# Optimization experiments

Hardware: AMD Instinct MI355X
Metric: run time of the kernel (lower is better)

## Reference

```python
import jax, jax.numpy as jnp
import numpy as np

N_REACHES = 4096
N_STEPS = 96
DT = 3600.0  # routing timestep (s), default from MuskingumCungeRouter


def safe_pow(base, exp, eps=1e-6):
    # AD-safe power: exp(e * log(max(b, eps)))
    return jnp.exp(exp * jnp.log(jnp.maximum(base, eps)))


def setup_inputs() -> dict:
    key = jax.random.key(0)
    ks = jax.random.split(key, 10)
    n, T = N_REACHES, N_STEPS
    u = lambda k, lo, hi, shape: jax.random.uniform(k, shape, minval=lo, maxval=hi)
    lateral_inflows = u(ks[0], 0.0, 5.0, (T, n))          # m^3/s lateral inflow
    initial_Q = u(ks[1], 0.1, 10.0, (n,))
    lengths = u(ks[2], 500.0, 10000.0, (n,))              # reach length (m)
    slopes = u(ks[3], 1e-4, 0.05, (n,))                   # bed slope
    manning_n = u(ks[4], 0.02, 0.08, (n,))
    width_coef = u(ks[5], 2.0, 10.0, (n,))
    width_exp = u(ks[6], 0.4, 0.6, (n,))                  # ~0.5 typical
    depth_coef = u(ks[7], 0.2, 0.6, (n,))
    depth_exp = u(ks[8], 0.25, 0.35, (n,))                # ~0.3 typical
    # Strictly lower-triangular sparse adjacency: reach i receives from j < i
    # (valid topological order), ~4 upstream links per reach on average.
    upstream_mask = jnp.tril(jax.random.uniform(ks[9], (n, n)) < (4.0 / n), k=-1)
    is_outlet = jnp.arange(n) == n - 1
    return dict(lateral_inflows=lateral_inflows, initial_Q=initial_Q,
                lengths=lengths, slopes=slopes, manning_n=manning_n,
                width_coef=width_coef, width_exp=width_exp,
                depth_coef=depth_coef, depth_exp=depth_exp,
                upstream_mask=upstream_mask, is_outlet=is_outlet)


def _mc_coeffs(Q, L, S, mn, wc, we, dc, de, dt):
    """Vectorized Muskingum-Cunge coefficients for all reaches.

    Faithful fusion of compute_channel_geometry -> compute_velocity_manning ->
    compute_celerity -> compute_muskingum_params. Q here is Q_ref = max(state.Q, 0.1),
    which only depends on the previous state, so hoisting out of the per-reach
    scan is mathematically identical to the original.
    """
    Qs = jnp.maximum(Q, 0.01)
    W = wc * safe_pow(Qs, we)
    D = dc * safe_pow(Qs, de)
    A = W * D
    R = A / (W + 2.0 * D)                      # hydraulic radius
    safe_S = jnp.maximum(S, 1e-6)
    V = (1.0 / jnp.maximum(mn, 1e-3)) * safe_pow(R, 2.0 / 3.0) * jnp.sqrt(safe_S)
    c = jnp.maximum((5.0 / 3.0) * V, 0.01)     # kinematic wave celerity
    K = jnp.maximum(L / c, dt * 0.1)
    X = jnp.clip(0.5 * (1.0 - Q / (W * c * safe_S * L + 1e-6)), 0.0, 0.5)
    den = 2.0 * K * (1.0 - X) + dt
    C0 = jnp.maximum((dt - 2.0 * K * X) / den, 0.0)
    C1 = jnp.maximum((dt + 2.0 * K * X) / den, 0.0)
    C2 = jnp.maximum((2.0 * K * (1.0 - X) - dt) / den, 0.0)
    tot = C0 + C1 + C2
    return C0 / tot, C1 / tot, C2 / tot


def _route(lateral_inflows, initial_Q, lengths, slopes, manning_n,
           width_coef, width_exp, depth_coef, depth_exp,
           upstream_mask, is_outlet, dt=DT):
    n = lengths.shape[0]

    def step(state, lateral):
        Q, Q_prev, I_prev = state
        Q_ref = jnp.maximum(Q, 0.1)
        C0, C1, C2 = _mc_coeffs(Q_ref, lengths, slopes, manning_n,
                                width_coef, width_exp, depth_coef, depth_exp, dt)

        # Sequential topological sweep: masked reduction over already-routed reaches.
        def process(Q_acc, i):
            upstream_Q = jnp.sum(jnp.where(upstream_mask[i], Q_acc, 0.0))
            I_curr = upstream_Q + lateral[i]
            Q_out = jnp.maximum(C0[i] * I_curr + C1[i] * I_prev[i] + C2[i] * Q_prev[i], 0.0)
            return Q_acc.at[i].set(Q_out), I_curr

        Q_final, I_all = jax.lax.scan(process, jnp.zeros(n, lateral.dtype), jnp.arange(n))
        outlet_Q = jnp.sum(jnp.where(is_outlet, Q_final, 0.0))
        return (Q_final, Q, I_all), outlet_Q

    init = (initial_Q, initial_Q, jnp.zeros(n, initial_Q.dtype))
    _, outlet_series = jax.lax.scan(step, init, lateral_inflows)
    return outlet_series  # [n_timesteps]


def reference(lateral_inflows, initial_Q, lengths, slopes, manning_n,
              width_coef, width_exp, depth_coef, depth_exp,
              upstream_mask, is_outlet):
    return _route(lateral_inflows, initial_Q, lengths, slopes, manning_n,
                  width_coef, width_exp, depth_coef, depth_exp,
                  upstream_mask, is_outlet)
```

## Files before the change

### kernel.cpp

```cpp
#include <hip/hip_runtime.h>

#define NR 4096
#define NT 96
#define NNZ_CAP 10240
#define SREM_CAP 4096
#define LONG_CAP 4096
#define WLDS 8
#define SSTR 4112
#define DHIST 32
#define DTSTEP 3600.0f
#define LOG2_1E6 -19.931568f

__device__ __forceinline__ float RCP(float x) { return __builtin_amdgcn_rcpf(x); }
__device__ __forceinline__ float EXP2(float x) { return __builtin_amdgcn_exp2f(x); }
__device__ __forceinline__ float LOG2(float x) { return __builtin_amdgcn_logf(x); }

__device__ __forceinline__ void phase_barrier() {
  asm volatile("s_waitcnt lgkmcnt(0) vmcnt(6)" ::: "memory");
  __builtin_amdgcn_s_barrier();
  asm volatile("" ::: "memory");
}

__global__ void mc_build(const int* __restrict__ mask, int* __restrict__ rowBase,
                         int* __restrict__ rowCnt, int* __restrict__ gctr,
                         unsigned short* __restrict__ cols) {
  __shared__ unsigned short tmp[80];
  __shared__ int baseS;
  int row = blockIdx.x;
  int lane = threadIdx.x;
  const int* rs = mask + (size_t)row * NR;
  int total = 0;
  for (int j0 = 0; j0 < NR; j0 += 64) {
    int j = j0 + lane;
    int pred = (rs[j] != 0);
    unsigned long long m = __ballot(pred);
    if (pred) {
      int pos = total + __popcll(m & ((1ull << lane) - 1ull));
      if (pos < 80) tmp[pos] = (unsigned short)j;
    }
    total += __popcll(m);
  }
  if (total > 80) total = 80;
  if (lane == 0) {
    int b = atomicAdd(gctr, total);
    rowBase[row] = b;
    rowCnt[row] = total;
    baseS = b;
  }
  __syncthreads();
  int base = baseS;
  for (int e = lane; e < total; e += 64) {
    int p = base + e;
    if (p < NNZ_CAP) cols[p] = tmp[e];
  }
}

__global__ __launch_bounds__(1024) void mc_prep(
    const int* __restrict__ rowBase, const int* __restrict__ rowCnt,
    const int* __restrict__ gctr, const unsigned short* __restrict__ colsOld,
    unsigned short* __restrict__ orderG, unsigned short* __restrict__ levNG,
    unsigned short* __restrict__ scolG, unsigned int* __restrict__ sremMeta,
    unsigned int* __restrict__ longMeta, unsigned short* __restrict__ sremG,
    unsigned short* __restrict__ longG, unsigned char* __restrict__ lsG,
    int* __restrict__ meta) {
  __shared__ unsigned short cols_s[NNZ_CAP];
  __shared__ unsigned char lev_s[NR];
  __shared__ unsigned short newid_s[NR];
  __shared__ unsigned short order_s[NR];
  __shared__ unsigned char lsrc_s[NR];
  __shared__ int cnt[1024];
  __shared__ int sbuf[1024];
  __shared__ int maxLevS, flagS;
  const int tid = threadIdx.x;
  int nnz = gctr[0];
  if (nnz > NNZ_CAP) nnz = NNZ_CAP;
  for (int e = tid; e < nnz; e += 1024) cols_s[e] = colsOld[e];

  int b_r[4], e_r[4];
#pragma unroll
  for (int k = 0; k < 4; ++k) {
    int i = 4 * tid + k;
    int b = rowBase[i];
    if (b > NNZ_CAP) b = NNZ_CAP;
    int e = b + rowCnt[i];
    if (e > NNZ_CAP) e = NNZ_CAP;
    b_r[k] = b;
    e_r[k] = e;
    lev_s[i] = 0;
    lsrc_s[i] = 0;
  }
  if (tid == 0) maxLevS = 0;
  __syncthreads();

  for (int pass = 0; pass < 48; ++pass) {
    if (tid == 0) flagS = 0;
    __syncthreads();
    int ch = 0;
#pragma unroll
    for (int k = 0; k < 4; ++k) {
      int i = 4 * tid + k;
      int lv = 0;
      for (int e = b_r[k]; e < e_r[k]; ++e) {
        int l2 = (int)lev_s[cols_s[e]] + 1;
        lv = lv > l2 ? lv : l2;
      }
      if (lv > 127) lv = 127;
      if (lv > (int)lev_s[i]) {
        lev_s[i] = (unsigned char)lv;
        ch = 1;
      }
    }
    if (ch) flagS = 1;
    __syncthreads();
    int done = (flagS == 0);
    __syncthreads();
    if (done) break;
  }
  int lm = 0;
#pragma unroll
  for (int k = 0; k < 4; ++k) {
    int l = lev_s[4 * tid + k];
    lm = lm > l ? lm : l;
  }
  atomicMax(&maxLevS, lm);
  __syncthreads();
  const int maxLev = maxLevS;
  if (tid == 0) {
    meta[0] = maxLev + 1;
    meta[2] = (maxLev >= DHIST) ? 1 : 0;
  }
  if (maxLev >= DHIST) {
#pragma unroll
    for (int k = 0; k < 4; ++k) {
      int i = 4 * tid + k;
      orderG[i] = (unsigned short)i;
      levNG[i] = (unsigned short)lev_s[i];
    }
    return;
  }

  cnt[tid] = 0;
  __syncthreads();
  int bkt_r[4];
#pragma unroll
  for (int k = 0; k < 4; ++k) {
    int i = 4 * tid + k;
    int d = e_r[k] - b_r[k];
    if (d > 31) d = 31;
    int bkt = ((int)lev_s[i]) * 32 + d;
    bkt_r[k] = bkt;
    atomicAdd(&cnt[bkt], 1);
  }
  __syncthreads();
  int v = cnt[tid];
  sbuf[tid] = v;
  __syncthreads();
  for (int off = 1; off < 1024; off <<= 1) {
    int add = tid >= off ? sbuf[tid - off] : 0;
    __syncthreads();
    sbuf[tid] += add;
    __syncthreads();
  }
  cnt[tid] = sbuf[tid] - v;
  __syncthreads();
#pragma unroll
  for (int k = 0; k < 4; ++k) {
    int i = 4 * tid + k;
    int pos = atomicAdd(&cnt[bkt_r[k]], 1);
    order_s[pos] = (unsigned short)i;
    newid_s[i] = (unsigned short)pos;
  }
  __syncthreads();

#pragma unroll
  for (int k = 0; k < 4; ++k) {
    int p = 4 * tid + k;
    int oldi = order_s[p];
    orderG[p] = (unsigned short)oldi;
    int lp = (int)lev_s[oldi];
    levNG[p] = (unsigned short)lp;
    int b = rowBase[oldi];
    if (b > NNZ_CAP) b = NNZ_CAP;
    int e = b + rowCnt[oldi];
    if (e > NNZ_CAP) e = NNZ_CAP;
    int nS = 0, nR = 0, nL = 0;
    for (int ee = b; ee < e; ++ee) {
      int lag = lp - (int)lev_s[cols_s[ee]];
      if (lag < WLDS) {
        if (nS < 4) ++nS; else ++nR;
      } else ++nL;
    }
    if (nR > 63) nR = 63;
    if (nL > 63) nL = 63;
    int sB = nR ? atomicAdd(&meta[4], nR) : 0;
    int lB = nL ? atomicAdd(&meta[5], nL) : 0;
    if (sB > SREM_CAP) sB = SREM_CAP;
    if (sB + nR > SREM_CAP) nR = SREM_CAP - sB;
    if (lB > LONG_CAP) lB = LONG_CAP;
    if (lB + nL > LONG_CAP) nL = LONG_CAP - lB;
    unsigned short sc[4] = {4096, 4096, 4096, 4096};
    int iS = 0, cR = 0, cL = 0;
    for (int ee = b; ee < e; ++ee) {
      int cOld = cols_s[ee];
      int cN = newid_s[cOld];
      int lag = lp - (int)lev_s[cOld];
      if (lag < WLDS) {
        if (iS < 4) sc[iS++] = (unsigned short)cN;
        else if (cR < nR) { sremG[sB + cR] = (unsigned short)cN; ++cR; }
      } else {
        if (cL < nL) { longG[lB + cL] = (unsigned short)cN; ++cL; }
        lsrc_s[cN] = 1;
      }
    }
    scolG[4 * p + 0] = sc[0];
    scolG[4 * p + 1] = sc[1];
    scolG[4 * p + 2] = sc[2];
    scolG[4 * p + 3] = sc[3];
    sremMeta[p] = (unsigned)sB | ((unsigned)nR << 20) | ((unsigned)iS << 26);
    longMeta[p] = (unsigned)lB | ((unsigned)nL << 20);
  }
  if (tid == 0) meta[1] = newid_s[NR - 1];
  __syncthreads();
#pragma unroll
  for (int k = 0; k < 4; ++k) {
    int p = 4 * tid + k;
    lsG[p] = lsrc_s[p];
  }
}

__global__ void mc_permlat(const float* __restrict__ lat,
                           const unsigned short* __restrict__ orderG,
                           float* __restrict__ latP) {
  int g = blockIdx.x * 256 + threadIdx.x;
  int t = g >> 12, p = g & 4095;
  latP[g] = lat[t * NR + orderG[p]];
}

__global__ __launch_bounds__(1024, 4) void mc_route(
    const float* __restrict__ lat, const float* __restrict__ latP,
    const float* __restrict__ initQ, const float* __restrict__ Lg,
    const float* __restrict__ Sg, const float* __restrict__ mng,
    const float* __restrict__ wcg, const float* __restrict__ weg,
    const float* __restrict__ dcg, const float* __restrict__ deg,
    const int* __restrict__ rowBase, const int* __restrict__ rowCnt,
    const unsigned short* __restrict__ colsOld,
    const unsigned short* __restrict__ orderG,
    const unsigned short* __restrict__ levNG,
    const unsigned short* __restrict__ scolG,
    const unsigned int* __restrict__ sremMeta,
    const unsigned int* __restrict__ longMeta,
    const unsigned short* __restrict__ sremG,
    const unsigned short* __restrict__ longG,
    const unsigned char* __restrict__ lsG, const int* __restrict__ meta,
    float* Qhist, float* __restrict__ out, int usePerm) {
  __shared__ float win_s[WLDS * SSTR];
  __shared__ unsigned short srem_s[SREM_CAP];
  __shared__ unsigned short long_s[LONG_CAP];
  const int tid = threadIdx.x;
  const int nlv = meta[0];
  const int fb = meta[2];
  const int outletNew = meta[1];
  const float* latB = usePerm ? latP : lat;

  if (!fb) {
    int sc_r[4][4];
    int lev_r[4], io_r[4], ls_r[4], wOff_r[4], nsc_r[4];
    unsigned int smeta_r[4], lmeta_r[4];
    const float* latp_r[4];
    float lwc_r[4], we_r[4], ldc_r[4], de_r[4], lvk_r[4], lgSL_r[4], L_r[4];
    float ip_r[4], q1_r[4], q2_r[4], latN_r[4];

    int nSrem = meta[4];
    if (nSrem > SREM_CAP) nSrem = SREM_CAP;
    int nLong = meta[5];
    if (nLong > LONG_CAP) nLong = LONG_CAP;
    for (int e = tid; e < nSrem; e += 1024) srem_s[e] = sremG[e];
    for (int e = tid; e < nLong; e += 1024) long_s[e] = longG[e];
    if (tid < WLDS) win_s[tid * SSTR + 4096] = 0.f;

#pragma unroll
    for (int k = 0; k < 4; ++k) {
      int p = tid + k * 1024;
      int oldi = orderG[p];
      lev_r[k] = (int)levNG[p];
      uint2 cc = *(const uint2*)(scolG + 4 * p);
      sc_r[k][0] = cc.x & 0xFFFFu;
      sc_r[k][1] = cc.x >> 16;
      sc_r[k][2] = cc.y & 0xFFFFu;
      sc_r[k][3] = cc.y >> 16;
      smeta_r[k] = sremMeta[p];
      nsc_r[k] = (int)(smeta_r[k] >> 26);
      lmeta_r[k] = longMeta[p];
      ls_r[k] = (int)lsG[p];
      io_r[k] = (p == outletNew);
      float Lv = Lg[oldi];
      float sS = fmaxf(Sg[oldi], 1e-6f);
      float mnv = fmaxf(mng[oldi], 1e-3f);
      lvk_r[k] = 0.7369656f + 0.5f * LOG2(sS) - LOG2(mnv);
      lgSL_r[k] = LOG2(sS * Lv);
      L_r[k] = Lv;
      lwc_r[k] = LOG2(wcg[oldi]);
      we_r[k] = weg[oldi];
      ldc_r[k] = LOG2(dcg[oldi]);
      de_r[k] = deg[oldi];
      float q0 = initQ[oldi];
      q1_r[k] = q0;
      q2_r[k] = q0;
      ip_r[k] = 0.f;
      wOff_r[k] = 0;
      latp_r[k] = latB + (usePerm ? p : oldi);
      latN_r[k] = *latp_r[k];
    }
    __syncthreads();

#define BODY(k, tt)                                                             \
  {                                                                             \
    const int p = tid + (k)*1024;                                               \
    const float latv = latN_r[k];                                               \
    latp_r[k] += ((tt) + 1 < NT) ? NR : 0;                                      \
    latN_r[k] = *latp_r[k];              \
    const int wB = wOff_r[k];                                                   \
    float v0 = win_s[wB + sc_r[k][0]];                                          \
    float v1 = win_s[wB + sc_r[k][1]];                                          \
    float v23 = 0.f;                                                            \
    if (nsc_r[k] > 2)                                                           \
      v23 = win_s[wB + sc_r[k][2]] + win_s[wB + sc_r[k][3]];                    \
    float ssum = 0.f;                                                           \
    const int sC = (int)((smeta_r[k] >> 20) & 63);                              \
    if (sC) {                                                                   \
      const int sB = (int)(smeta_r[k] & 0xFFFFFu);                              \
      for (int e = 0; e < sC; ++e) ssum += win_s[wB + srem_s[sB + e]];          \
    }                                                                           \
    float lsum = 0.f;                                                           \
    const int lC = (int)(lmeta_r[k] >> 20);                                     \
    if (lC) {                                                                   \
      const int lB = (int)(lmeta_r[k] & 0xFFFFFu);                              \
      const float* qb = Qhist + (((tt)&31) << 12);                              \
      for (int e = 0; e < lC; ++e) lsum += qb[long_s[lB + e]];                  \
    }                                                                           \
    float Qref = fmaxf(q1_r[k], 0.1f);                                          \
    float lq = LOG2(Qref);                                                      \
    float lgW = fmaf(we_r[k], lq, lwc_r[k]);                                    \
    float W = EXP2(lgW);                                                        \
    float aD = fmaf(de_r[k], lq, ldc_r[k]);                                     \
    float Dd = EXP2(aD);                                                        \
    float lgR = fmaxf(lgW + aD - LOG2(fmaf(2.f, Dd, W)), LOG2_1E6);             \
    float lgc = fmaf(0.66666667f, lgR, lvk_r[k]);                               \
    float K = fmaxf(L_r[k] * EXP2(-lgc), 360.f);                                \
    float ratio = EXP2(lq - lgW - lgc - lgSL_r[k]);                             \
    float X = fmaxf(fmaf(-0.5f, ratio, 0.5f), 0.f);                             \
    float twoK = K + K;                                                         \
    float twoKX = twoK * X;                                                     \
    float C0 = fmaxf(DTSTEP - twoKX, 0.f);                                      \
    float C1 = DTSTEP + twoKX;                                                  \
    float C2 = fmaxf(twoK - twoKX - DTSTEP, 0.f);                               \
    float inv = RCP(C0 + C1 + C2);                                              \
    float sup = ((v0 + v1) + v23) + (ssum + lsum);                              \
    float Icurr = sup + latv;                                                   \
    float Qout = fmaxf((C0 * Icurr + C1 * ip_r[k] + C2 * q2_r[k]) * inv, 0.f);  \
    win_s[wB + p] = Qout;                                                       \
    if (ls_r[k]) Qhist[(((tt)&31) << 12) | p] = Qout;                           \
    if (io_r[k]) out[tt] = Qout;                                                \
    ip_r[k] = Icurr;                                                            \
    q2_r[k] = q1_r[k];                                                          \
    q1_r[k] = Qout;                                                             \
    wOff_r[k] = (wOff_r[k] == (WLDS - 1) * SSTR) ? 0 : wOff_r[k] + SSTR;        \
  }

#define BODYC(k, s)                                                            \
  {                                                                            \
    int t = (s)-lev_r[k];                                                      \
    if ((unsigned)t < (unsigned)NT) BODY(k, t)                                 \
  }

    for (int s = 0; s < nlv - 1; ++s) {
#pragma unroll
      for (int k = 0; k < 4; ++k) BODYC(k, s);
      phase_barrier();
    }
    for (int s = nlv - 1; s < NT; ++s) {
#pragma unroll
      for (int k = 0; k < 4; ++k) {
        int t = s - lev_r[k];
        BODY(k, t);
      }
      phase_barrier();
    }
    for (int s = NT; s < NT + nlv - 1; ++s) {
#pragma unroll
      for (int k = 0; k < 4; ++k) BODYC(k, s);
      phase_barrier();
    }
  } else {
    unsigned short* colsF = (unsigned short*)win_s;
    int b_r[4], e_r[4], lev_r[4];
    float lwc_r[4], we_r[4], ldc_r[4], de_r[4], lvk_r[4], SL_r[4], L_r[4];
    float ip_r[4], q1_r[4], q2_r[4];
    for (int e = tid; e < NNZ_CAP; e += 1024) colsF[e] = colsOld[e];
#pragma unroll
    for (int k = 0; k < 4; ++k) {
      int i = tid + k * 1024;
      lev_r[k] = (int)levNG[i];
      int b = rowBase[i];
      if (b > NNZ_CAP) b = NNZ_CAP;
      int e = b + rowCnt[i];
      if (e > NNZ_CAP) e = NNZ_CAP;
      b_r[k] = b;
      e_r[k] = e;
      float Lv = Lg[i];
      float sS = fmaxf(Sg[i], 1e-6f);
      float mnv = fmaxf(mng[i], 1e-3f);
      lvk_r[k] = 0.7369656f + 0.5f * LOG2(sS) - LOG2(mnv);
      SL_r[k] = sS * Lv;
      L_r[k] = Lv;
      lwc_r[k] = LOG2(wcg[i]);
      we_r[k] = weg[i];
      ldc_r[k] = LOG2(dcg[i]);
      de_r[k] = deg[i];
      float q0 = initQ[i];
      q1_r[k] = q0;
      q2_r[k] = q0;
      ip_r[k] = 0.f;
    }
    __syncthreads();
    for (int t = 0; t < NT; ++t) {
      for (int l = 0; l < nlv; ++l) {
#pragma unroll
        for (int k = 0; k < 4; ++k) {
          if (lev_r[k] == l) {
            int i = tid + k * 1024;
            float latv = lat[t * NR + i];
            float Qref = fmaxf(q1_r[k], 0.1f);
            float lq = LOG2(Qref);
            float lgW = fmaf(we_r[k], lq, lwc_r[k]);
            float W = EXP2(lgW);
            float aD = fmaf(de_r[k], lq, ldc_r[k]);
            float Dd = EXP2(aD);
            float lgR = fmaxf(lgW + aD - LOG2(fmaf(2.f, Dd, W)), LOG2_1E6);
            float c = fmaxf(EXP2(fmaf(0.66666667f, lgR, lvk_r[k])), 0.01f);
            float K = fmaxf(L_r[k] * RCP(c), 360.f);
            float X =
                fmaxf(0.5f - 0.5f * Qref * RCP(fmaf(W * c, SL_r[k], 1e-6f)), 0.f);
            float twoKX = 2.f * K * X;
            float C0 = fmaxf(DTSTEP - twoKX, 0.f);
            float C1 = DTSTEP + twoKX;
            float C2 = fmaxf(2.f * K - twoKX - DTSTEP, 0.f);
            float inv = RCP(C0 + C1 + C2);
            float sup = 0.f;
            for (int e = b_r[k]; e < e_r[k]; ++e) sup += Qhist[colsF[e]];
            float Icurr = sup + latv;
            float Qout =
                fmaxf((C0 * Icurr + C1 * ip_r[k] + C2 * q2_r[k]) * inv, 0.f);
            Qhist[i] = Qout;
            ip_r[k] = Icurr;
            q2_r[k] = q1_r[k];
            q1_r[k] = Qout;
            if (i == NR - 1) out[t] = Qout;
          }
        }
        __syncthreads();
      }
    }
  }
}

extern "C" void kernel_launch(void* const* d_in, const int* in_sizes, int n_in,
                              void* d_out, int out_size, void* d_ws, size_t ws_size,
                              hipStream_t stream) {
  const float* lat = (const float*)d_in[0];
  const float* iQ = (const float*)d_in[1];
  const float* Lg = (const float*)d_in[2];
  const float* Sg = (const float*)d_in[3];
  const float* mng = (const float*)d_in[4];
  const float* wcg = (const float*)d_in[5];
  const float* weg = (const float*)d_in[6];
  const float* dcg = (const float*)d_in[7];
  const float* deg = (const float*)d_in[8];
  const int* mask = (const int*)d_in[9];
  float* out = (float*)d_out;

  char* w = (char*)d_ws;
  int* rowBase = (int*)w;                        w += NR * 4;
  int* rowCnt = (int*)w;                         w += NR * 4;
  int* gctr = (int*)w;                           w += 16;
  int* meta = (int*)w;                           w += 32;
  unsigned short* colsOld = (unsigned short*)w;  w += NNZ_CAP * 2;
  unsigned short* orderG = (unsigned short*)w;   w += NR * 2;
  unsigned short* levNG = (unsigned short*)w;    w += NR * 2;
  unsigned short* scolG = (unsigned short*)w;    w += NR * 4 * 2;
  unsigned int* sremMeta = (unsigned int*)w;     w += NR * 4;
  unsigned int* longMeta = (unsigned int*)w;     w += NR * 4;
  unsigned short* sremG = (unsigned short*)w;    w += SREM_CAP * 2;
  unsigned short* longG = (unsigned short*)w;    w += LONG_CAP * 2;
  unsigned char* lsG = (unsigned char*)w;        w += NR;
  w += 16 - ((size_t)w & 15);
  float* Qhist = (float*)w;                      w += (size_t)DHIST * NR * 4;
  float* latP = (float*)w;                       w += (size_t)NT * NR * 4;
  size_t need = (size_t)(w - (char*)d_ws);
  int usePerm = (ws_size >= need) ? 1 : 0;

  hipMemsetAsync(gctr, 0, 48, stream);
  mc_build<<<NR, 64, 0, stream>>>(mask, rowBase, rowCnt, gctr, colsOld);
  mc_prep<<<1, 1024, 0, stream>>>(rowBase, rowCnt, gctr, colsOld, orderG, levNG,
                                  scolG, sremMeta, longMeta, sremG, longG, lsG,
                                  meta);
  if (usePerm)
    mc_permlat<<<(NT * NR) / 256, 256, 0, stream>>>(lat, orderG, latP);
  mc_route<<<1, 1024, 0, stream>>>(lat, latP, iQ, Lg, Sg, mng, wcg, weg, dcg,
                                   deg, rowBase, rowCnt, colsOld, orderG, levNG,
                                   scolG, sremMeta, longMeta, sremG, longG, lsG,
                                   meta, Qhist, out, usePerm);
}
```

Before: 465.1 us.

## Process two timesteps per barrier phase with doubled level skew

```diff
diff --git a/kernel.cpp b/kernel.cpp
--- a/kernel.cpp
+++ b/kernel.cpp
@@ -7,7 +7,8 @@
 #define LONG_CAP 4096
 #define WLDS 8
 #define SSTR 4112
-#define DHIST 32
+#define DHIST 64
+#define SHORTLAG 3
 #define DTSTEP 3600.0f
 #define LOG2_1E6 -19.931568f
 
@@ -16,7 +17,7 @@
 __device__ __forceinline__ float LOG2(float x) { return __builtin_amdgcn_logf(x); }
 
 __device__ __forceinline__ void phase_barrier() {
-  asm volatile("s_waitcnt lgkmcnt(0) vmcnt(6)" ::: "memory");
+  asm volatile("s_waitcnt lgkmcnt(0) vmcnt(8)" ::: "memory");
   __builtin_amdgcn_s_barrier();
   asm volatile("" ::: "memory");
 }
@@ -70,11 +71,13 @@
   __shared__ unsigned char lsrc_s[NR];
   __shared__ int cnt[1024];
   __shared__ int sbuf[1024];
-  __shared__ int maxLevS, flagS;
+  __shared__ int flagA[40];
+  __shared__ int maxLevS;
   const int tid = threadIdx.x;
   int nnz = gctr[0];
   if (nnz > NNZ_CAP) nnz = NNZ_CAP;
   for (int e = tid; e < nnz; e += 1024) cols_s[e] = colsOld[e];
+  for (int i = tid; i < 40; i += 1024) flagA[i] = 0;
 
   int b_r[4], e_r[4];
 #pragma unroll
@@ -92,9 +95,7 @@
   if (tid == 0) maxLevS = 0;
   __syncthreads();
 
-  for (int pass = 0; pass < 48; ++pass) {
-    if (tid == 0) flagS = 0;
-    __syncthreads();
+  for (int pass = 0; pass < 34; ++pass) {
     int ch = 0;
 #pragma unroll
     for (int k = 0; k < 4; ++k) {
@@ -104,17 +105,15 @@
         int l2 = (int)lev_s[cols_s[e]] + 1;
         lv = lv > l2 ? lv : l2;
       }
-      if (lv > 127) lv = 127;
+      if (lv > 60) lv = 60;
       if (lv > (int)lev_s[i]) {
         lev_s[i] = (unsigned char)lv;
         ch = 1;
       }
     }
-    if (ch) flagS = 1;
+    if (ch) flagA[pass] = 1;
     __syncthreads();
-    int done = (flagS == 0);
-    __syncthreads();
-    if (done) break;
+    if (flagA[pass] == 0) break;
   }
   int lm = 0;
 #pragma unroll
@@ -127,9 +126,9 @@
   const int maxLev = maxLevS;
   if (tid == 0) {
     meta[0] = maxLev + 1;
-    meta[2] = (maxLev >= DHIST) ? 1 : 0;
-  }
-  if (maxLev >= DHIST) {
+    meta[2] = (maxLev >= 32) ? 1 : 0;
+  }
+  if (maxLev >= 32) {
 #pragma unroll
     for (int k = 0; k < 4; ++k) {
       int i = 4 * tid + k;
@@ -186,7 +185,7 @@
     int nS = 0, nR = 0, nL = 0;
     for (int ee = b; ee < e; ++ee) {
       int lag = lp - (int)lev_s[cols_s[ee]];
-      if (lag < WLDS) {
+      if (lag <= SHORTLAG) {
         if (nS < 4) ++nS; else ++nR;
       } else ++nL;
     }
@@ -204,7 +203,7 @@
       int cOld = cols_s[ee];
       int cN = newid_s[cOld];
       int lag = lp - (int)lev_s[cOld];
-      if (lag < WLDS) {
+      if (lag <= SHORTLAG) {
         if (iS < 4) sc[iS++] = (unsigned short)cN;
         else if (cR < nR) { sremG[sB + cR] = (unsigned short)cN; ++cR; }
       } else {
@@ -266,9 +265,9 @@
     int sc_r[4][4];
     int lev_r[4], io_r[4], ls_r[4], wOff_r[4], nsc_r[4];
     unsigned int smeta_r[4], lmeta_r[4];
-    const float* latp_r[4];
+    const float* latcol_r[4];
     float lwc_r[4], we_r[4], ldc_r[4], de_r[4], lvk_r[4], lgSL_r[4], L_r[4];
-    float ip_r[4], q1_r[4], q2_r[4], latN_r[4];
+    float ip_r[4], q1_r[4], q2_r[4], latE_r[4], latO_r[4];
 
     int nSrem = meta[4];
     if (nSrem > SREM_CAP) nSrem = SREM_CAP;
@@ -308,17 +307,19 @@
       q2_r[k] = q0;
       ip_r[k] = 0.f;
       wOff_r[k] = 0;
-      latp_r[k] = latB + (usePerm ? p : oldi);
-      latN_r[k] = *latp_r[k];
+      latcol_r[k] = latB + (usePerm ? p : oldi);
+      latE_r[k] = latcol_r[k][0];
+      latO_r[k] = latcol_r[k][NR];
     }
     __syncthreads();
 
-#define BODY(k, tt)                                                             \
+#define BODY(k, tt, LATR)                                                       \
   {                                                                             \
     const int p = tid + (k)*1024;                                               \
-    const float latv = latN_r[k];                                               \
-    latp_r[k] += ((tt) + 1 < NT) ? NR : 0;                                      \
-    latN_r[k] = *latp_r[k];              \
+    const float latv = LATR[k];                                                 \
+    int tn = (tt) + 2;                                                          \
+    tn = tn < NT ? tn : NT - 1;                                                 \
+    LATR[k] = latcol_r[k][tn << 12];                                            \
     const int wB = wOff_r[k];                                                   \
     float v0 = win_s[wB + sc_r[k][0]];                                          \
     float v1 = win_s[wB + sc_r[k][1]];                                          \
@@ -335,7 +336,7 @@
     const int lC = (int)(lmeta_r[k] >> 20);                                     \
     if (lC) {                                                                   \
       const int lB = (int)(lmeta_r[k] & 0xFFFFFu);                              \
-      const float* qb = Qhist + (((tt)&31) << 12);                              \
+      const float* qb = Qhist + (((tt) & (DHIST - 1)) << 12);                   \
       for (int e = 0; e < lC; ++e) lsum += qb[long_s[lB + e]];                  \
     }                                                                           \
     float Qref = fmaxf(q1_r[k], 0.1f);                                          \
@@ -359,7 +360,7 @@
     float Icurr = sup + latv;                                                   \
     float Qout = fmaxf((C0 * Icurr + C1 * ip_r[k] + C2 * q2_r[k]) * inv, 0.f);  \
     win_s[wB + p] = Qout;                                                       \
-    if (ls_r[k]) Qhist[(((tt)&31) << 12) | p] = Qout;                           \
+    if (ls_r[k]) Qhist[((((tt) & (DHIST - 1)) << 12)) | p] = Qout;              \
     if (io_r[k]) out[tt] = Qout;                                                \
     ip_r[k] = Icurr;                                                            \
     q2_r[k] = q1_r[k];                                                          \
@@ -367,28 +368,25 @@
     wOff_r[k] = (wOff_r[k] == (WLDS - 1) * SSTR) ? 0 : wOff_r[k] + SSTR;        \
   }
 
-#define BODYC(k, s)                                                            \
-  {                                                                            \
-    int t = (s)-lev_r[k];                                                      \
-    if ((unsigned)t < (unsigned)NT) BODY(k, t)                                 \
-  }
-
-    for (int s = 0; s < nlv - 1; ++s) {
-#pragma unroll
-      for (int k = 0; k < 4; ++k) BODYC(k, s);
-      phase_barrier();
-    }
-    for (int s = nlv - 1; s < NT; ++s) {
-#pragma unroll
-      for (int k = 0; k < 4; ++k) {
-        int t = s - lev_r[k];
-        BODY(k, t);
+    const int ML = nlv - 1;
+    const int lastD = NT - 1 + 2 * ML;
+    for (int d0 = 0; d0 <= lastD; d0 += 2) {
+      if (d0 >= 2 * ML && d0 <= NT - 2) {
+#pragma unroll
+        for (int k = 0; k < 4; ++k) {
+          int t0 = d0 - 2 * lev_r[k];
+          BODY(k, t0, latE_r);
+          BODY(k, t0 + 1, latO_r);
+        }
+      } else {
+#pragma unroll
+        for (int k = 0; k < 4; ++k) {
+          int t0 = d0 - 2 * lev_r[k];
+          if ((unsigned)t0 < (unsigned)NT) BODY(k, t0, latE_r);
+          int t1 = t0 + 1;
+          if ((unsigned)t1 < (unsigned)NT) BODY(k, t1, latO_r);
+        }
       }
-      phase_barrier();
-    }
-    for (int s = NT; s < NT + nlv - 1; ++s) {
-#pragma unroll
-      for (int k = 0; k < 4; ++k) BODYC(k, s);
       phase_barrier();
     }
   } else {
```

Result: slower. 745.4 us (+60.3%).
